# Performance work log

Hardware: AMD Instinct MI355X
Metric: run time of the kernel (lower is better)

## Reference

```python
import jax, jax.numpy as jnp
import numpy as np
from jax import lax

TAU = 2.0  # SynapseFilter time constant (learnable=False)


def setup_inputs() -> dict:
    key = jax.random.key(0)
    T, N, C, D_out = 64, 16, 128, 256
    k1, k2 = jax.random.split(key)
    x = jax.random.uniform(k1, (T, N, C, 2), dtype=jnp.float32)  # spike-like input (T,N,C,2)
    # matches torch init: _log_delay = log(linspace(1e-7, 1, D_out)).view(-1,1)
    log_delay = jnp.log(jnp.linspace(1e-7, 1.0, D_out, dtype=jnp.float32)).reshape(D_out, 1)
    log_weight = jnp.log(jnp.float32(2.0))
    # uniform noise replacing torch.bernoulli(p) (u < p  <=>  bernoulli(p))
    noise = jax.random.uniform(k2, (N, C, D_out, 2), dtype=jnp.float32)
    return {"x": x, "log_delay": log_delay, "log_weight": log_weight, "noise": noise}


def reference(x, log_delay, log_weight, noise):
    T, N, C, _ = x.shape
    D_out = log_delay.shape[0]

    # delay property: cat([exp(log_delay), flip(exp(log_delay))], dim=1) -> (D_out, 2)
    d = jnp.exp(log_delay)                      # (D_out, 1)
    delay = jnp.concatenate([d, d[::-1]], axis=1)  # (D_out, 2)

    # stochastic rounding of T * delay, broadcast to (N, C, D_out, 2)
    scaled = jnp.broadcast_to((T * delay)[None, None], (N, C, D_out, 2))
    fl = jnp.floor(scaled)
    rounded = fl + (noise < (scaled - fl)).astype(scaled.dtype)

    # clamp(max = T - 1 - argmax over time). argmax of the repeated tensor equals
    # argmax of x broadcast over D_out, so compute it cheaply on x.
    am = jnp.argmax(x, axis=0)                  # (N, C, 2)
    max_d = (T - 1 - am)[:, :, None, :]         # (N, C, 1, 2)
    rd = jnp.minimum(rounded.astype(jnp.int32), max_d.astype(jnp.int32))  # (N,C,D_out,2)

    # circular delay-line shift: out[t] = in[(t - delay) mod T]
    out_rep = jnp.broadcast_to(x[:, :, :, None, :], (T, N, C, D_out, 2))
    t_idx = jnp.arange(T, dtype=jnp.int32)[:, None, None, None, None]
    idx = (t_idx - rd[None]) % T                # (T, N, C, D_out, 2)
    shifted = jnp.take_along_axis(out_rep, idx, axis=0)

    # SynapseFilter (multi-step): y_t = y_{t-1} * (1 - 1/tau) + x_t, y_{-1}=0
    decay = jnp.float32(1.0 - 1.0 / TAU)

    def step(carry, xt):
        carry = carry * decay + xt
        return carry, carry

    _, y = lax.scan(step, jnp.zeros_like(shifted[0]), shifted)  # (T,N,C,D_out,2)

    # scale by weight = exp(log_weight), sum over D_in=2
    out = (y * jnp.exp(log_weight)).sum(axis=-1)  # (T, N, C, D_out)
    return out
```

## Files before the change

kernel.cpp:

```cpp
#include <hip/hip_runtime.h>
#include <math.h>

#define T_STEPS 64
#define D_OUT 256
#define NCB 4

typedef float vfloat4 __attribute__((ext_vector_type(4)));

__global__ __launch_bounds__(256) void jeffress_kernel(
    const float* __restrict__ x,
    const float* __restrict__ log_delay,
    const float* __restrict__ log_weight,
    const float* __restrict__ noise,
    float* __restrict__ out,
    int NC)
{
    __shared__ float  xs0[NCB][T_STEPS];
    __shared__ float  xs1[NCB][T_STEPS];
    __shared__ double fracd[D_OUT];
    __shared__ int    flo[D_OUT];
    __shared__ int    maxd[NCB][2];

    const int tid = threadIdx.x;
    const int nc_base = blockIdx.x * NCB;
    const int lnc = tid >> 6;
    const int jj  = tid & 63;
    const int nc  = nc_base + lnc;

    {
        int t = tid >> 2;
        int l = tid & 3;
        const float* xp = x + ((size_t)t * NC + nc_base + l) * 2;
        xs0[l][t] = xp[0];
        xs1[l][t] = xp[1];
    }
    {
        double s = (double)T_STEPS * exp((double)log_delay[tid]);
        double f = floor(s);
        fracd[tid] = s - f;
        flo[tid]   = (int)f;
    }
    __syncthreads();

    if (tid < NCB * 2) {
        int l = tid >> 1, i = tid & 1;
        const float* xsrc = i ? xs1[l] : xs0[l];
        float best = xsrc[0]; int bi = 0;
        for (int t = 1; t < T_STEPS; ++t) {
            float v = xsrc[t];
            if (v > best) { best = v; bi = t; }
        }
        maxd[l][i] = (T_STEPS - 1) - bi;
    }
    __syncthreads();

    const float* nptr = noise + ((size_t)nc * D_OUT + 4 * jj) * 2;
    float4 na = *(const float4*)(nptr);
    float4 nb = *(const float4*)(nptr + 4);
    float n0i[4] = { na.x, na.z, nb.x, nb.z };
    float n1i[4] = { na.y, na.w, nb.y, nb.w };

    const int md0 = maxd[lnc][0];
    const int md1 = maxd[lnc][1];

    int rd0[4], rd1[4];
    #pragma unroll
    for (int c = 0; c < 4; ++c) {
        int j  = 4 * jj + c;
        int jf = (D_OUT - 1) - j;
        int r0 = flo[j]  + (((double)n0i[c] < fracd[j])  ? 1 : 0);
        int r1 = flo[jf] + (((double)n1i[c] < fracd[jf]) ? 1 : 0);
        rd0[c] = min(r0, md0);
        rd1[c] = min(r1, md1);
    }

    const float w = (float)exp((double)log_weight[0]);

    float y0[4] = {0.f, 0.f, 0.f, 0.f};
    float y1[4] = {0.f, 0.f, 0.f, 0.f};
    const float* xr0 = xs0[lnc];
    const float* xr1 = xs1[lnc];
    float* op = out + ((size_t)nc) * D_OUT + 4 * jj;
    const size_t ostride = (size_t)NC * D_OUT;

    #pragma unroll
    for (int t = 0; t < T_STEPS; ++t) {
        vfloat4 o;
        #pragma unroll
        for (int c = 0; c < 4; ++c) {
            y0[c] = y0[c] * 0.5f + xr0[(t - rd0[c]) & (T_STEPS - 1)];
            y1[c] = y1[c] * 0.5f + xr1[(t - rd1[c]) & (T_STEPS - 1)];
            o[c] = (y0[c] + y1[c]) * w;
        }
        __builtin_nontemporal_store(o, (vfloat4*)(op + (size_t)t * ostride));
    }
}

extern "C" void kernel_launch(void* const* d_in, const int* in_sizes, int n_in,
                              void* d_out, int out_size, void* d_ws, size_t ws_size,
                              hipStream_t stream) {
    const float* x          = (const float*)d_in[0];
    const float* log_delay  = (const float*)d_in[1];
    const float* log_weight = (const float*)d_in[2];
    const float* noise      = (const float*)d_in[3];
    float* out = (float*)d_out;

    const int NC = in_sizes[3] / (D_OUT * 2);

    jeffress_kernel<<<NC / NCB, 256, 0, stream>>>(x, log_delay, log_weight, noise, out, NC);
}
```

Measured before the change: 148.9 us.

## Split time axis across waves, one (n,c) per block with recompute prefix

Each block now handles a single (n,c) pair, and its four waves split the 64 time steps into 16-step chunks. Each wave recomputes the filter recurrence over the earlier steps without storing them, then emits its own chunk. The grid is four times larger and launch bounds request higher occupancy, aiming for more parallelism and less serial latency per thread. In exchange it adds redundant recurrence work and per-block setup (the log_delay exp and argmax) per (n,c), and it swaps the nontemporal stores for plain stores.

After: 148.2 us. No clear change (-0.5%).

```diff
diff --git a/kernel.cpp b/kernel.cpp
--- a/kernel.cpp
+++ b/kernel.cpp
@@ -3,11 +3,10 @@
 
 #define T_STEPS 64
 #define D_OUT 256
-#define NCB 4
 
 typedef float vfloat4 __attribute__((ext_vector_type(4)));
 
-__global__ __launch_bounds__(256) void jeffress_kernel(
+__global__ __launch_bounds__(256, 8) void jeffress_kernel(
     const float* __restrict__ x,
     const float* __restrict__ log_delay,
     const float* __restrict__ log_weight,
@@ -15,24 +14,21 @@
     float* __restrict__ out,
     int NC)
 {
-    __shared__ float  xs0[NCB][T_STEPS];
-    __shared__ float  xs1[NCB][T_STEPS];
+    __shared__ float  xs0[T_STEPS];
+    __shared__ float  xs1[T_STEPS];
     __shared__ double fracd[D_OUT];
     __shared__ int    flo[D_OUT];
-    __shared__ int    maxd[NCB][2];
+    __shared__ int    maxd[2];
 
     const int tid = threadIdx.x;
-    const int nc_base = blockIdx.x * NCB;
-    const int lnc = tid >> 6;
+    const int nc  = blockIdx.x;
+    const int wv  = tid >> 6;
     const int jj  = tid & 63;
-    const int nc  = nc_base + lnc;
 
-    {
-        int t = tid >> 2;
-        int l = tid & 3;
-        const float* xp = x + ((size_t)t * NC + nc_base + l) * 2;
-        xs0[l][t] = xp[0];
-        xs1[l][t] = xp[1];
+    if (tid < T_STEPS) {
+        const float* xp = x + ((size_t)tid * NC + nc) * 2;
+        xs0[tid] = xp[0];
+        xs1[tid] = xp[1];
     }
     {
         double s = (double)T_STEPS * exp((double)log_delay[tid]);
@@ -42,15 +38,14 @@
     }
     __syncthreads();
 
-    if (tid < NCB * 2) {
-        int l = tid >> 1, i = tid & 1;
-        const float* xsrc = i ? xs1[l] : xs0[l];
+    if (tid < 2) {
+        const float* xsrc = tid ? xs1 : xs0;
         float best = xsrc[0]; int bi = 0;
         for (int t = 1; t < T_STEPS; ++t) {
             float v = xsrc[t];
             if (v > best) { best = v; bi = t; }
         }
-        maxd[l][i] = (T_STEPS - 1) - bi;
+        maxd[tid] = (T_STEPS - 1) - bi;
     }
     __syncthreads();
 
@@ -59,9 +54,7 @@
     float4 nb = *(const float4*)(nptr + 4);
     float n0i[4] = { na.x, na.z, nb.x, nb.z };
     float n1i[4] = { na.y, na.w, nb.y, nb.w };
-
-    const int md0 = maxd[lnc][0];
-    const int md1 = maxd[lnc][1];
+    const int md0 = maxd[0], md1 = maxd[1];
 
     int rd0[4], rd1[4];
     #pragma unroll
@@ -78,21 +71,30 @@
 
     float y0[4] = {0.f, 0.f, 0.f, 0.f};
     float y1[4] = {0.f, 0.f, 0.f, 0.f};
-    const float* xr0 = xs0[lnc];
-    const float* xr1 = xs1[lnc];
-    float* op = out + ((size_t)nc) * D_OUT + 4 * jj;
+    const int t0 = wv * 16;
+
+    #pragma unroll 16
+    for (int t = 0; t < t0; ++t) {
+        #pragma unroll
+        for (int c = 0; c < 4; ++c) {
+            y0[c] = y0[c] * 0.5f + xs0[(t - rd0[c]) & (T_STEPS - 1)];
+            y1[c] = y1[c] * 0.5f + xs1[(t - rd1[c]) & (T_STEPS - 1)];
+        }
+    }
+
+    float* op = out + (size_t)nc * D_OUT + 4 * jj;
     const size_t ostride = (size_t)NC * D_OUT;
-
     #pragma unroll
-    for (int t = 0; t < T_STEPS; ++t) {
+    for (int k = 0; k < 16; ++k) {
+        int t = t0 + k;
         vfloat4 o;
         #pragma unroll
         for (int c = 0; c < 4; ++c) {
-            y0[c] = y0[c] * 0.5f + xr0[(t - rd0[c]) & (T_STEPS - 1)];
-            y1[c] = y1[c] * 0.5f + xr1[(t - rd1[c]) & (T_STEPS - 1)];
+            y0[c] = y0[c] * 0.5f + xs0[(t - rd0[c]) & (T_STEPS - 1)];
+            y1[c] = y1[c] * 0.5f + xs1[(t - rd1[c]) & (T_STEPS - 1)];
             o[c] = (y0[c] + y1[c]) * w;
         }
-        __builtin_nontemporal_store(o, (vfloat4*)(op + (size_t)t * ostride));
+        *(vfloat4*)(op + (size_t)t * ostride) = o;
     }
 }
 
@@ -107,5 +109,5 @@
 
     const int NC = in_sizes[3] / (D_OUT * 2);
 
-    jeffress_kernel<<<NC / NCB, 256, 0, stream>>>(x, log_delay, log_weight, noise, out, NC);
+    jeffress_kernel<<<NC, 256, 0, stream>>>(x, log_delay, log_weight, noise, out, NC);
 }
```
